# Optimization experiments

Hardware: AMD Instinct MI355X
Metric: run time of the kernel (lower is better)

Reference implementation:

```python
import jax, jax.numpy as jnp
import numpy as np

N, M, D, P = 4096, 8192, 512, 4
TEMP = 0.1  # SimCLR temperature


def setup_inputs() -> dict:
    key = jax.random.key(0)
    k1, k2, k3, k4 = jax.random.split(key, 4)
    queries = jax.random.normal(k1, (N, D), dtype=jnp.float32)
    keys = jax.random.normal(k2, (M, D), dtype=jnp.float32)
    # positives in lower half, ignores in upper half -> disjoint, no all--inf rows
    positive_indices = jax.random.randint(k3, (N, P), 0, M // 2)
    ignore_indices = jax.random.randint(k4, (N, P), M // 2, M)
    return dict(queries=queries, keys=keys,
                positive_indices=positive_indices, ignore_indices=ignore_indices)


def reference(queries, keys, positive_indices, ignore_indices):
    n, m = queries.shape[0], keys.shape[0]
    # score_fn = dot-product similarity, divided by temperature -> [N, M]
    scores = jnp.matmul(queries, keys.T) / TEMP
    rows = jnp.arange(n)[:, None]
    # scatter per-row index lists into boolean masks (duplicates collapse, as in torch)
    pos_mask = jnp.zeros((n, m), dtype=bool).at[rows, positive_indices].set(True)
    ign_mask = jnp.zeros((n, m), dtype=bool).at[rows, ignore_indices].set(True)
    neg_inf = jnp.array(-jnp.inf, dtype=scores.dtype)
    scores_m = jnp.where(ign_mask, neg_inf, scores)  # masked_fill(ignore, -inf)
    # scatter_logsumexp over positives == row-wise logsumexp restricted to pos_mask
    pos_lse = jax.nn.logsumexp(jnp.where(pos_mask, scores_m, neg_inf), axis=1)
    logp = pos_lse - jax.nn.logsumexp(scores_m, axis=1)
    loss = -jnp.sum(logp)
    preds = jnp.argmax(scores_m, axis=1)  # [N]
    corrects = jnp.any(positive_indices == preds[:, None], axis=1)  # [N] bool
    return (loss, corrects)
```

## Files before the change

kernel.cpp:

```cpp
#include <hip/hip_runtime.h>
#include <math.h>

#define N_Q 4096
#define M_K 8192
#define D_DIM 512
#define P_IDX 4
#define INV_TEMP 10.0f

#define NCHUNK 128

typedef __attribute__((ext_vector_type(8))) _Float16 f16x8;
typedef __attribute__((ext_vector_type(16))) float f32x16;

__global__ __launch_bounds__(256)
void pack_f16(const float* __restrict__ Q, const float* __restrict__ K,
              _Float16* __restrict__ Pq, _Float16* __restrict__ Pk,
              int qunits, int totunits)
{
    const int wunit = blockIdx.x * 4 + (threadIdx.x >> 6);
    if (wunit >= totunits) return;
    const bool isq = (wunit < qunits);
    const int u = isq ? wunit : wunit - qunits;
    const float* X = isq ? Q : K;
    _Float16* P = isq ? Pq : Pk;
    const float scale = isq ? INV_TEMP : 1.0f;
    const int rb = u >> 5, ks = u & 31;
    const int lane = threadIdx.x & 63;
    const int hi = lane >> 5, lx = lane & 31;
    const int row = rb * 32 + lx;
    const float4* src = (const float4*)(X + (size_t)row * D_DIM + ks * 16 + hi * 8);
    float4 v0 = src[0], v1 = src[1];
    f16x8 o;
    o[0] = (_Float16)(v0.x * scale); o[1] = (_Float16)(v0.y * scale);
    o[2] = (_Float16)(v0.z * scale); o[3] = (_Float16)(v0.w * scale);
    o[4] = (_Float16)(v1.x * scale); o[5] = (_Float16)(v1.y * scale);
    o[6] = (_Float16)(v1.z * scale); o[7] = (_Float16)(v1.w * scale);
    ((f16x8*)P)[(size_t)u * 64 + lane] = o;
}

#define MFMA_QUARTET(A0, A1, B0, B1)                                            \
    __builtin_amdgcn_s_setprio(1);                                              \
    acc[0][0] = __builtin_amdgcn_mfma_f32_32x32x16_f16(A0, B0, acc[0][0], 0, 0, 0); \
    acc[0][1] = __builtin_amdgcn_mfma_f32_32x32x16_f16(A0, B1, acc[0][1], 0, 0, 0); \
    acc[1][0] = __builtin_amdgcn_mfma_f32_32x32x16_f16(A1, B0, acc[1][0], 0, 0, 0); \
    acc[1][1] = __builtin_amdgcn_mfma_f32_32x32x16_f16(A1, B1, acc[1][1], 0, 0, 0); \
    __builtin_amdgcn_s_setprio(0);

__global__ __launch_bounds__(256)
void scores_mfma(const _Float16* __restrict__ Qp, const _Float16* __restrict__ Kp,
                 const int* __restrict__ ign, float4* __restrict__ part)
{
    const int tid = threadIdx.x;
    const int lane = tid & 63;
    const int wave = tid >> 6;
    const int wr = wave >> 1, wc = wave & 1;
    const int hi = lane >> 5, lx = lane & 31;
    const int bx = blockIdx.x;
    const int by = blockIdx.y;

    const f16x8* Kp8 = (const f16x8*)Kp;
    const f16x8* Qp8 = (const f16x8*)Qp;
    const f16x8* A0p = Kp8 + ((size_t)(bx * 4 + wr * 2 + 0) * 32) * 64 + lane;
    const f16x8* A1p = Kp8 + ((size_t)(bx * 4 + wr * 2 + 1) * 32) * 64 + lane;
    const f16x8* B0p = Qp8 + ((size_t)(by * 4 + wc * 2 + 0) * 32) * 64 + lane;
    const f16x8* B1p = Qp8 + ((size_t)(by * 4 + wc * 2 + 1) * 32) * 64 + lane;

    f32x16 acc[2][2];
#pragma unroll
    for (int i = 0; i < 2; ++i)
#pragma unroll
        for (int j = 0; j < 2; ++j) acc[i][j] = (f32x16)0.f;

    f16x8 rA0 = A0p[0],   rA1 = A1p[0],   rB0 = B0p[0],   rB1 = B1p[0];
    f16x8 sA0 = A0p[64],  sA1 = A1p[64],  sB0 = B0p[64],  sB1 = B1p[64];
    f16x8 tA0 = A0p[128], tA1 = A1p[128], tB0 = B0p[128], tB1 = B1p[128];
    f16x8 uA0 = A0p[192], uA1 = A1p[192], uB0 = B0p[192], uB1 = B1p[192];

    for (int ks = 0; ks < 32; ks += 4) {
        MFMA_QUARTET(rA0, rA1, rB0, rB1)
        if (ks + 4 < 32) {
            const int o = (ks + 4) * 64;
            rA0 = A0p[o]; rA1 = A1p[o]; rB0 = B0p[o]; rB1 = B1p[o];
        }
        MFMA_QUARTET(sA0, sA1, sB0, sB1)
        if (ks + 5 < 32) {
            const int o = (ks + 5) * 64;
            sA0 = A0p[o]; sA1 = A1p[o]; sB0 = B0p[o]; sB1 = B1p[o];
        }
        MFMA_QUARTET(tA0, tA1, tB0, tB1)
        if (ks + 6 < 32) {
            const int o = (ks + 6) * 64;
            tA0 = A0p[o]; tA1 = A1p[o]; tB0 = B0p[o]; tB1 = B1p[o];
        }
        MFMA_QUARTET(uA0, uA1, uB0, uB1)
        if (ks + 7 < 32) {
            const int o = (ks + 7) * 64;
            uA0 = A0p[o]; uA1 = A1p[o]; uB0 = B0p[o]; uB1 = B1p[o];
        }
    }

    const int kbase = bx * 128 + wr * 64 + 4 * hi;
    const int chunk = bx * 2 + wr;
#pragma unroll
    for (int j = 0; j < 2; ++j) {
        const int qrow = by * 128 + wc * 64 + j * 32 + lx;
        const int4 ig = ((const int4*)ign)[qrow];
        float bm = -INFINITY; int bi = 0x7fffffff;
#pragma unroll
        for (int i = 0; i < 2; ++i) {
#pragma unroll
            for (int r = 0; r < 16; ++r) {
                const int col = kbase + i * 32 + (r & 3) + 8 * (r >> 2);
                float x = acc[i][j][r];
                if (col == ig.x || col == ig.y || col == ig.z || col == ig.w)
                    x = -INFINITY;
                acc[i][j][r] = x;
                if (x > bm || (x == bm && col < bi)) { bm = x; bi = col; }
            }
        }
        float se = 0.f;
#pragma unroll
        for (int i = 0; i < 2; ++i)
#pragma unroll
            for (int r = 0; r < 16; ++r)
                se += __expf(acc[i][j][r] - bm);

        const float obm = __shfl_xor(bm, 32);
        const float ose = __shfl_xor(se, 32);
        const int   obi = __shfl_xor(bi, 32);
        const float nm = fmaxf(bm, obm);
        se = se * __expf(bm - nm) + ose * __expf(obm - nm);
        if (obm > bm || (obm == bm && obi < bi)) bi = obi;
        bm = nm;
        if (hi == 0)
            part[(size_t)qrow * NCHUNK + chunk] =
                make_float4(bm, se, __int_as_float(bi), 0.f);
    }
}

__global__ __launch_bounds__(256)
void combine_kernel(const float4* __restrict__ part,
                    const float* __restrict__ Q, const float* __restrict__ K,
                    const int* __restrict__ pos,
                    float* __restrict__ logp, float* __restrict__ corrects)
{
    const int row = blockIdx.x * 4 + (threadIdx.x >> 6);
    const int lane = threadIdx.x & 63;

    float4 p0 = part[(size_t)row * NCHUNK + lane];
    float m = p0.x, s = p0.y, av = p0.x;
    int ai = __float_as_int(p0.z);
    {
        float4 p = part[(size_t)row * NCHUNK + 64 + lane];
        int oi = __float_as_int(p.z);
        float nm = fmaxf(m, p.x);
        s = s * expf(m - nm) + p.y * expf(p.x - nm);
        m = nm;
        if (p.x > av || (p.x == av && oi < ai)) { av = p.x; ai = oi; }
    }

#pragma unroll
    for (int off = 32; off >= 1; off >>= 1) {
        float om = __shfl_xor(m, off);
        float os = __shfl_xor(s, off);
        float oav = __shfl_xor(av, off);
        int oi = __shfl_xor(ai, off);
        float nm = fmaxf(m, om);
        s = s * expf(m - nm) + os * expf(om - nm);
        m = nm;
        if (oav > av || (oav == av && oi < ai)) { av = oav; ai = oi; }
    }
    float lse = m + logf(s);

    int pi[4];
#pragma unroll
    for (int p = 0; p < 4; ++p) pi[p] = pos[row * P_IDX + p];

    const float4* q4 = (const float4*)(Q + (size_t)row * D_DIM);
    float4 qa = q4[lane * 2], qb = q4[lane * 2 + 1];
    float d[4];
#pragma unroll
    for (int p = 0; p < 4; ++p) {
        const float4* k4 = (const float4*)(K + (size_t)pi[p] * D_DIM);
        float4 ka = k4[lane * 2], kb = k4[lane * 2 + 1];
        d[p] = qa.x * ka.x + qa.y * ka.y + qa.z * ka.z + qa.w * ka.w
             + qb.x * kb.x + qb.y * kb.y + qb.z * kb.z + qb.w * kb.w;
    }
#pragma unroll
    for (int off = 32; off >= 1; off >>= 1) {
#pragma unroll
        for (int p = 0; p < 4; ++p) d[p] += __shfl_xor(d[p], off);
    }

    if (lane == 0) {
        float ps[4];
#pragma unroll
        for (int p = 0; p < 4; ++p) ps[p] = d[p] * INV_TEMP;
        const bool v1 = (pi[1] != pi[0]);
        const bool v2 = (pi[2] != pi[0]) && (pi[2] != pi[1]);
        const bool v3 = (pi[3] != pi[0]) && (pi[3] != pi[1]) && (pi[3] != pi[2]);
        float pm = ps[0];
        if (v1) pm = fmaxf(pm, ps[1]);
        if (v2) pm = fmaxf(pm, ps[2]);
        if (v3) pm = fmaxf(pm, ps[3]);
        float pse = expf(ps[0] - pm);
        if (v1) pse += expf(ps[1] - pm);
        if (v2) pse += expf(ps[2] - pm);
        if (v3) pse += expf(ps[3] - pm);
        float pos_lse = pm + logf(pse);
        logp[row] = pos_lse - lse;
        bool corr = (ai == pi[0]) || (ai == pi[1]) || (ai == pi[2]) || (ai == pi[3]);
        corrects[row] = corr ? 1.0f : 0.0f;
    }
}

__global__ __launch_bounds__(256)
void loss_kernel(const float* __restrict__ logp, float* __restrict__ out)
{
    __shared__ float sm[256];
    const int t = threadIdx.x;
    float s = 0.f;
    for (int i = t; i < N_Q; i += 256) s += logp[i];
    sm[t] = s;
    __syncthreads();
    for (int off = 128; off >= 1; off >>= 1) {
        if (t < off) sm[t] += sm[t + off];
        __syncthreads();
    }
    if (t == 0) out[0] = -sm[0];
}

extern "C" void kernel_launch(void* const* d_in, const int* in_sizes, int n_in,
                              void* d_out, int out_size, void* d_ws, size_t ws_size,
                              hipStream_t stream)
{
    const float* Q = (const float*)d_in[0];
    const float* K = (const float*)d_in[1];
    const int* pos = (const int*)d_in[2];
    const int* ign = (const int*)d_in[3];
    float* out = (float*)d_out;

    _Float16* Qp = (_Float16*)d_ws;
    _Float16* Kp = Qp + (size_t)N_Q * D_DIM;
    float4* part = (float4*)(Kp + (size_t)M_K * D_DIM);
    float* logp = (float*)(part + (size_t)N_Q * NCHUNK);

    const int qunits = N_Q / 32 * 32;
    const int totunits = qunits + M_K / 32 * 32;
    pack_f16<<<totunits / 4, 256, 0, stream>>>(Q, K, Qp, Kp, qunits, totunits);

    dim3 gridA(M_K / 128, N_Q / 128);
    scores_mfma<<<gridA, 256, 0, stream>>>(Qp, Kp, ign, part);
    combine_kernel<<<N_Q / 4, 256, 0, stream>>>(part, Q, K, pos, logp, out + 1);
    loss_kernel<<<1, 256, 0, stream>>>(logp, out);
}
```

Before: 74.87 us.

## Stage key tile in LDS and loop each block over four query tiles

Each score block now copies a 64-key by 512-dim fp16 slice into shared memory once with global_load_lds. It then reuses that slice across four 128-query tiles, streaming query fragments from global memory with register prefetch. This cuts redundant global/L2 reads of key data, but each block holds 64KB of LDS, which limits occupancy, and each wave now keeps only two accumulators. The combine kernel also switches to fast __expf/__logf intrinsics.

```diff
diff --git a/kernel.cpp b/kernel.cpp
--- a/kernel.cpp
+++ b/kernel.cpp
@@ -38,92 +38,116 @@
     ((f16x8*)P)[(size_t)u * 64 + lane] = o;
 }
 
-#define MFMA_QUARTET(A0, A1, B0, B1)                                            \
-    __builtin_amdgcn_s_setprio(1);                                              \
-    acc[0][0] = __builtin_amdgcn_mfma_f32_32x32x16_f16(A0, B0, acc[0][0], 0, 0, 0); \
-    acc[0][1] = __builtin_amdgcn_mfma_f32_32x32x16_f16(A0, B1, acc[0][1], 0, 0, 0); \
-    acc[1][0] = __builtin_amdgcn_mfma_f32_32x32x16_f16(A1, B0, acc[1][0], 0, 0, 0); \
-    acc[1][1] = __builtin_amdgcn_mfma_f32_32x32x16_f16(A1, B1, acc[1][1], 0, 0, 0); \
-    __builtin_amdgcn_s_setprio(0);
+__device__ __forceinline__ void gload16(const void* g, const void* l) {
+    __builtin_amdgcn_global_load_lds(
+        (const __attribute__((address_space(1))) unsigned int*)g,
+        (__attribute__((address_space(3))) unsigned int*)l, 16, 0, 0);
+}
 
 __global__ __launch_bounds__(256)
 void scores_mfma(const _Float16* __restrict__ Qp, const _Float16* __restrict__ Kp,
                  const int* __restrict__ ign, float4* __restrict__ part)
 {
+    __shared__ __align__(16) _Float16 As[32768];
+
     const int tid = threadIdx.x;
     const int lane = tid & 63;
-    const int wave = tid >> 6;
-    const int wr = wave >> 1, wc = wave & 1;
+    const int w = tid >> 6;
     const int hi = lane >> 5, lx = lane & 31;
     const int bx = blockIdx.x;
-    const int by = blockIdx.y;
+    const int slice = blockIdx.y;
 
     const f16x8* Kp8 = (const f16x8*)Kp;
     const f16x8* Qp8 = (const f16x8*)Qp;
-    const f16x8* A0p = Kp8 + ((size_t)(bx * 4 + wr * 2 + 0) * 32) * 64 + lane;
-    const f16x8* A1p = Kp8 + ((size_t)(bx * 4 + wr * 2 + 1) * 32) * 64 + lane;
-    const f16x8* B0p = Qp8 + ((size_t)(by * 4 + wc * 2 + 0) * 32) * 64 + lane;
-    const f16x8* B1p = Qp8 + ((size_t)(by * 4 + wc * 2 + 1) * 32) * 64 + lane;
-
-    f32x16 acc[2][2];
-#pragma unroll
-    for (int i = 0; i < 2; ++i)
-#pragma unroll
-        for (int j = 0; j < 2; ++j) acc[i][j] = (f32x16)0.f;
-
-    f16x8 rA0 = A0p[0],   rA1 = A1p[0],   rB0 = B0p[0],   rB1 = B1p[0];
-    f16x8 sA0 = A0p[64],  sA1 = A1p[64],  sB0 = B0p[64],  sB1 = B1p[64];
-    f16x8 tA0 = A0p[128], tA1 = A1p[128], tB0 = B0p[128], tB1 = B1p[128];
-    f16x8 uA0 = A0p[192], uA1 = A1p[192], uB0 = B0p[192], uB1 = B1p[192];
-
-    for (int ks = 0; ks < 32; ks += 4) {
-        MFMA_QUARTET(rA0, rA1, rB0, rB1)
-        if (ks + 4 < 32) {
-            const int o = (ks + 4) * 64;
-            rA0 = A0p[o]; rA1 = A1p[o]; rB0 = B0p[o]; rB1 = B1p[o];
+    f16x8* As8 = (f16x8*)As;
+
+    {
+        const f16x8* src = Kp8 + (size_t)bx * 4096;
+#pragma unroll
+        for (int it = 0; it < 16; ++it)
+            gload16(src + it * 256 + tid, As8 + it * 256 + tid);
+    }
+    __syncthreads();
+
+    int qrb = (slice * 4) * 4 + w;
+    const f16x8* Bp = Qp8 + (size_t)qrb * 2048 + lane;
+    f16x8 bR = Bp[0], bS = Bp[64], bT = Bp[128], bU = Bp[192];
+
+    for (int t = 0; t < 4; ++t) {
+        const int by = slice * 4 + t;
+        f32x16 acc0 = (f32x16)0.f, acc1 = (f32x16)0.f;
+
+#pragma unroll
+        for (int ks = 0; ks < 32; ks += 4) {
+            {
+                f16x8 a0 = As8[(ks) * 64 + lane];
+                f16x8 a1 = As8[(32 + ks) * 64 + lane];
+                __builtin_amdgcn_s_setprio(1);
+                acc0 = __builtin_amdgcn_mfma_f32_32x32x16_f16(a0, bR, acc0, 0, 0, 0);
+                acc1 = __builtin_amdgcn_mfma_f32_32x32x16_f16(a1, bR, acc1, 0, 0, 0);
+                __builtin_amdgcn_s_setprio(0);
+            }
+            if (ks + 4 < 32) bR = Bp[(ks + 4) * 64];
+            {
+                f16x8 a0 = As8[(ks + 1) * 64 + lane];
+                f16x8 a1 = As8[(33 + ks) * 64 + lane];
+                __builtin_amdgcn_s_setprio(1);
+                acc0 = __builtin_amdgcn_mfma_f32_32x32x16_f16(a0, bS, acc0, 0, 0, 0);
+                acc1 = __builtin_amdgcn_mfma_f32_32x32x16_f16(a1, bS, acc1, 0, 0, 0);
+                __builtin_amdgcn_s_setprio(0);
+            }
+            if (ks + 5 < 32) bS = Bp[(ks + 5) * 64];
+            {
+                f16x8 a0 = As8[(ks + 2) * 64 + lane];
+                f16x8 a1 = As8[(34 + ks) * 64 + lane];
+                __builtin_amdgcn_s_setprio(1);
+                acc0 = __builtin_amdgcn_mfma_f32_32x32x16_f16(a0, bT, acc0, 0, 0, 0);
+                acc1 = __builtin_amdgcn_mfma_f32_32x32x16_f16(a1, bT, acc1, 0, 0, 0);
+                __builtin_amdgcn_s_setprio(0);
+            }
+            if (ks + 6 < 32) bT = Bp[(ks + 6) * 64];
+            {
+                f16x8 a0 = As8[(ks + 3) * 64 + lane];
+                f16x8 a1 = As8[(35 + ks) * 64 + lane];
+                __builtin_amdgcn_s_setprio(1);
+                acc0 = __builtin_amdgcn_mfma_f32_32x32x16_f16(a0, bU, acc0, 0, 0, 0);
+                acc1 = __builtin_amdgcn_mfma_f32_32x32x16_f16(a1, bU, acc1, 0, 0, 0);
+                __builtin_amdgcn_s_setprio(0);
+            }
+            if (ks + 7 < 32) bU = Bp[(ks + 7) * 64];
         }
-        MFMA_QUARTET(sA0, sA1, sB0, sB1)
-        if (ks + 5 < 32) {
-            const int o = (ks + 5) * 64;
-            sA0 = A0p[o]; sA1 = A1p[o]; sB0 = B0p[o]; sB1 = B1p[o];
-        }
-        MFMA_QUARTET(tA0, tA1, tB0, tB1)
-        if (ks + 6 < 32) {
-            const int o = (ks + 6) * 64;
-            tA0 = A0p[o]; tA1 = A1p[o]; tB0 = B0p[o]; tB1 = B1p[o];
-        }
-        MFMA_QUARTET(uA0, uA1, uB0, uB1)
-        if (ks + 7 < 32) {
-            const int o = (ks + 7) * 64;
-            uA0 = A0p[o]; uA1 = A1p[o]; uB0 = B0p[o]; uB1 = B1p[o];
-        }
-    }
-
-    const int kbase = bx * 128 + wr * 64 + 4 * hi;
-    const int chunk = bx * 2 + wr;
-#pragma unroll
-    for (int j = 0; j < 2; ++j) {
-        const int qrow = by * 128 + wc * 64 + j * 32 + lx;
+
+        const f16x8* Bpn = Bp + 8192;
+        if (t < 3) { bR = Bpn[0]; bS = Bpn[64]; bT = Bpn[128]; bU = Bpn[192]; }
+        Bp = Bpn;
+
+        const int qrow = by * 128 + w * 32 + lx;
+        const int kbase = bx * 64 + 4 * hi;
         const int4 ig = ((const int4*)ign)[qrow];
         float bm = -INFINITY; int bi = 0x7fffffff;
 #pragma unroll
-        for (int i = 0; i < 2; ++i) {
-#pragma unroll
-            for (int r = 0; r < 16; ++r) {
-                const int col = kbase + i * 32 + (r & 3) + 8 * (r >> 2);
-                float x = acc[i][j][r];
-                if (col == ig.x || col == ig.y || col == ig.z || col == ig.w)
-                    x = -INFINITY;
-                acc[i][j][r] = x;
-                if (x > bm || (x == bm && col < bi)) { bm = x; bi = col; }
-            }
+        for (int r = 0; r < 16; ++r) {
+            const int col = kbase + (r & 3) + 8 * (r >> 2);
+            float x = acc0[r];
+            if (col == ig.x || col == ig.y || col == ig.z || col == ig.w)
+                x = -INFINITY;
+            acc0[r] = x;
+            if (x > bm || (x == bm && col < bi)) { bm = x; bi = col; }
+        }
+#pragma unroll
+        for (int r = 0; r < 16; ++r) {
+            const int col = kbase + 32 + (r & 3) + 8 * (r >> 2);
+            float x = acc1[r];
+            if (col == ig.x || col == ig.y || col == ig.z || col == ig.w)
+                x = -INFINITY;
+            acc1[r] = x;
+            if (x > bm || (x == bm && col < bi)) { bm = x; bi = col; }
         }
         float se = 0.f;
 #pragma unroll
-        for (int i = 0; i < 2; ++i)
-#pragma unroll
-            for (int r = 0; r < 16; ++r)
-                se += __expf(acc[i][j][r] - bm);
+        for (int r = 0; r < 16; ++r) se += __expf(acc0[r] - bm);
+#pragma unroll
+        for (int r = 0; r < 16; ++r) se += __expf(acc1[r] - bm);
 
         const float obm = __shfl_xor(bm, 32);
         const float ose = __shfl_xor(se, 32);
@@ -133,7 +157,7 @@
         if (obm > bm || (obm == bm && obi < bi)) bi = obi;
         bm = nm;
         if (hi == 0)
-            part[(size_t)qrow * NCHUNK + chunk] =
+            part[(size_t)qrow * NCHUNK + bx] =
                 make_float4(bm, se, __int_as_float(bi), 0.f);
     }
 }
@@ -154,7 +178,7 @@
         float4 p = part[(size_t)row * NCHUNK + 64 + lane];
         int oi = __float_as_int(p.z);
         float nm = fmaxf(m, p.x);
-        s = s * expf(m - nm) + p.y * expf(p.x - nm);
+        s = s * __expf(m - nm) + p.y * __expf(p.x - nm);
         m = nm;
         if (p.x > av || (p.x == av && oi < ai)) { av = p.x; ai = oi; }
     }
@@ -166,11 +190,11 @@
         float oav = __shfl_xor(av, off);
         int oi = __shfl_xor(ai, off);
         float nm = fmaxf(m, om);
-        s = s * expf(m - nm) + os * expf(om - nm);
+        s = s * __expf(m - nm) + os * __expf(om - nm);
         m = nm;
         if (oav > av || (oav == av && oi < ai)) { av = oav; ai = oi; }
     }
-    float lse = m + logf(s);
+    float lse = m + __logf(s);
 
     int pi[4];
 #pragma unroll
@@ -203,11 +227,11 @@
         if (v1) pm = fmaxf(pm, ps[1]);
         if (v2) pm = fmaxf(pm, ps[2]);
         if (v3) pm = fmaxf(pm, ps[3]);
-        float pse = expf(ps[0] - pm);
-        if (v1) pse += expf(ps[1] - pm);
-        if (v2) pse += expf(ps[2] - pm);
-        if (v3) pse += expf(ps[3] - pm);
-        float pos_lse = pm + logf(pse);
+        float pse = __expf(ps[0] - pm);
+        if (v1) pse += __expf(ps[1] - pm);
+        if (v2) pse += __expf(ps[2] - pm);
+        if (v3) pse += __expf(ps[3] - pm);
+        float pos_lse = pm + __logf(pse);
         logp[row] = pos_lse - lse;
         bool corr = (ai == pi[0]) || (ai == pi[1]) || (ai == pi[2]) || (ai == pi[3]);
         corrects[row] = corr ? 1.0f : 0.0f;
@@ -249,7 +273,7 @@
     const int totunits = qunits + M_K / 32 * 32;
     pack_f16<<<totunits / 4, 256, 0, stream>>>(Q, K, Qp, Kp, qunits, totunits);
 
-    dim3 gridA(M_K / 128, N_Q / 128);
+    dim3 gridA(M_K / 64, 8);
     scores_mfma<<<gridA, 256, 0, stream>>>(Qp, Kp, ign, part);
     combine_kernel<<<N_Q / 4, 256, 0, stream>>>(part, Q, K, pos, logp, out + 1);
     loss_kernel<<<1, 256, 0, stream>>>(logp, out);
```

Result: slower. 79.69 us (+6.4%).
